# Kernel tuning notes

Hardware: AMD Instinct MI355X
Metric: run time of the kernel (lower is better)

Reference implementation:

```python
import jax, jax.numpy as jnp
import numpy as np

DIR_EDGES = [(0,1),(0,2),(0,3),(0,4),(0,13),(0,15),(3,5),(5,6),(4,7),(7,8),(1,9),(9,10),(2,11),(11,12),(13,14),(15,16)]
BP_EDGES = [(1,0),(1,2),(1,3),(1,4),(1,5)]
BODY_PARTS = [[13,14,15,16],[0,3,4],[1,9,10],[2,11,12],[5,6],[7,8]]
V1, V2 = 17, 6           # dir-vec graph nodes, body-part graph nodes
F1 = 16                  # st_gcn output channels
MAX_BP = 4               # max_body_part_edges
NOISE_DIM = 64
EPS = 1e-5


def build_A(num_node, edges, max_hop=2, center=0):
    """ST-GCN 'spatial' partition strategy -> (2*max_hop+1, V, V) float32."""
    adj = np.zeros((num_node, num_node))
    for i, j in edges:
        adj[i, j] = 1.0
        adj[j, i] = 1.0
    hop_dis = np.full((num_node, num_node), np.inf)
    powers = [np.linalg.matrix_power(adj + np.eye(num_node), d) for d in range(max_hop + 1)]
    arrive = np.stack(powers) > 0
    for d in range(max_hop, -1, -1):
        hop_dis[arrive[d]] = d
    adjacency = np.zeros((num_node, num_node))
    for hop in range(max_hop + 1):
        adjacency[hop_dis == hop] = 1.0
    Dl = adjacency.sum(0)
    Dn = np.zeros((num_node, num_node))
    for i in range(num_node):
        if Dl[i] > 0:
            Dn[i, i] = Dl[i] ** -1
    na = adjacency @ Dn
    parts = []
    for hop in range(max_hop + 1):
        a_root = np.zeros((num_node, num_node))
        a_close = np.zeros_like(a_root)
        a_far = np.zeros_like(a_root)
        for i in range(num_node):
            for j in range(num_node):
                if hop_dis[j, i] == hop:
                    if hop_dis[j, center] == hop_dis[i, center]:
                        a_root[j, i] = na[j, i]
                    elif hop_dis[j, center] > hop_dis[i, center]:
                        a_close[j, i] = na[j, i]
                    else:
                        a_far[j, i] = na[j, i]
        if hop == 0:
            parts.append(a_root)
        else:
            parts.append(a_root + a_close)
            parts.append(a_far)
    return np.stack(parts).astype(np.float32)


def _bn_params(k, c):
    k1, k2, k3, k4 = jax.random.split(k, 4)
    gamma = 1.0 + 0.1 * jax.random.normal(k1, (c,), dtype=jnp.float32)
    beta = 0.1 * jax.random.normal(k2, (c,), dtype=jnp.float32)
    mean = 0.1 * jax.random.normal(k3, (c,), dtype=jnp.float32)
    var = 1.0 + 0.1 * jax.random.uniform(k4, (c,), dtype=jnp.float32)
    return gamma, beta, mean, var


def setup_inputs() -> dict:
    key = jax.random.key(0)
    ks = jax.random.split(key, 12)
    n, t = 16, 2048
    poses = jax.random.normal(ks[0], (n, t, V1 * 3), dtype=jnp.float32)
    A1 = jnp.asarray(build_A(V1, DIR_EDGES, max_hop=2, center=0))  # (5,17,17)
    A2 = jnp.asarray(build_A(V2, BP_EDGES, max_hop=2, center=0))   # (5,6,6)
    K = 5
    w1 = 0.05 * jax.random.normal(ks[1], (F1 * K, 3, 9, 5), dtype=jnp.float32)
    b1 = 0.05 * jax.random.normal(ks[2], (F1 * K,), dtype=jnp.float32)
    w2 = 0.05 * jax.random.normal(ks[3], (F1 * K, MAX_BP * F1, 9, 3), dtype=jnp.float32)
    b2 = 0.05 * jax.random.normal(ks[4], (F1 * K,), dtype=jnp.float32)
    w3 = 0.05 * jax.random.normal(ks[5], (16, F1 * V2, 5), dtype=jnp.float32)
    b3 = 0.05 * jax.random.normal(ks[6], (16,), dtype=jnp.float32)
    w4 = 0.05 * jax.random.normal(ks[7], (NOISE_DIM, 16, 3), dtype=jnp.float32)
    b4 = 0.05 * jax.random.normal(ks[8], (NOISE_DIM,), dtype=jnp.float32)
    g1, be1, m1, v1 = _bn_params(ks[9], F1 * V1)
    g2, be2, m2, v2 = _bn_params(ks[10], F1 * V2)
    kk = jax.random.split(ks[11], 2)
    g3, be3, m3, v3 = _bn_params(kk[0], 16)
    g4, be4, m4, v4 = _bn_params(kk[1], NOISE_DIM)
    return dict(poses=poses, A1=A1, A2=A2, w1=w1, b1=b1, g1=g1, be1=be1, m1=m1, v1=v1,
                w2=w2, b2=b2, g2=g2, be2=be2, m2=m2, v2=v2,
                w3=w3, b3=b3, g3=g3, be3=be3, m3=m3, v3=v3,
                w4=w4, b4=b4, g4=g4, be4=be4, m4=m4, v4=v4)


def _bn(x, g, b, m, v):
    # x: (n, C, t), eval-mode BatchNorm1d
    s = (g * jax.lax.rsqrt(v + EPS))
    return (x - m[None, :, None]) * s[None, :, None] + b[None, :, None]


def _conv2d(x, w, b, pad):
    y = jax.lax.conv_general_dilated(x, w, (1, 1), [(pad[0], pad[0]), (pad[1], pad[1])],
                                     dimension_numbers=('NCHW', 'OIHW', 'NCHW'))
    return y + b[None, :, None, None]


def _conv1d(x, w, b, pad):
    y = jax.lax.conv_general_dilated(x, w, (1,), [(pad, pad)],
                                     dimension_numbers=('NCH', 'OIH', 'NCH'))
    return y + b[None, :, None]


def _leaky(x):
    return jax.nn.leaky_relu(x, 0.01)


def reference(poses, A1, A2, w1, b1, g1, be1, m1, v1, w2, b2, g2, be2, m2, v2,
              w3, b3, g3, be3, m3, v3, w4, b4, g4, be4, m4, v4):
    n, t, _ = poses.shape
    K = A1.shape[0]
    # (n, 3, t, V1)
    x = jnp.transpose(poses.reshape(n, t, V1, 3), (0, 3, 1, 2))
    # st_gcn1: 2D conv over (t, v) then graph-partition einsum
    y = _conv2d(x, w1, b1, (4, 2)).reshape(n, K, F1, t, V1)
    f1 = jnp.einsum('nkctv,kvw->nctw', y, A1)            # (n, F1, t, V1)
    # bn1 on flattened (F1*V1) channels
    z = jnp.transpose(f1, (0, 1, 3, 2)).reshape(n, F1 * V1, t)
    z = _bn(z, g1, be1, m1, v1)
    f1bn = jnp.transpose(z.reshape(n, F1, V1, t), (0, 1, 3, 2))  # (n, F1, t, V1)
    # body-part gather/pad assembly -> (n, t, MAX_BP*F1, V2)
    cols = []
    for idxs in BODY_PARTS:
        g = f1bn[:, :, :, jnp.asarray(idxs)]             # (n, F1, t, L)
        g = jnp.transpose(g, (0, 2, 1, 3)).reshape(n, t, -1)  # (n, t, F1*L)
        cols.append(jnp.pad(g, ((0, 0), (0, 0), (0, MAX_BP * F1 - g.shape[-1]))))
    f2_in = jnp.transpose(jnp.stack(cols, axis=-1), (0, 2, 1, 3))  # (n, 64, t, V2)
    # st_gcn2
    y2 = _conv2d(f2_in, w2, b2, (4, 1)).reshape(n, K, F1, t, V2)
    f2 = jnp.einsum('nkctv,kvw->nctw', y2, A2)           # (n, F1, t, V2)
    z2 = jnp.transpose(f2, (0, 1, 3, 2)).reshape(n, F1 * V2, t)
    z2 = _bn(z2, g2, be2, m2, v2)
    f2bn = jnp.transpose(z2.reshape(n, F1, V2, t), (0, 1, 3, 2))   # (n, F1, t, V2)
    # (n, F1*V2, t)
    f3_in = jnp.transpose(jnp.transpose(f2bn, (0, 2, 1, 3)).reshape(n, t, -1), (0, 2, 1))
    f3 = _leaky(_bn(_conv1d(f3_in, w3, b3, 2), g3, be3, m3, v3))
    f4 = _leaky(_bn(_conv1d(f3, w4, b4, 1), g4, be4, m4, v4))
    return jnp.transpose(f4, (0, 2, 1))                  # (n, t, noise_dim)
```

## Files before the change

kernel.cpp:

```cpp
#include <hip/hip_runtime.h>
#include <stdint.h>

typedef unsigned short u16;
typedef __attribute__((ext_vector_type(8))) __bf16 bf16x8;
typedef __attribute__((ext_vector_type(8))) u16 u16x8;
typedef __attribute__((ext_vector_type(4))) float f32x4;

#define T_LEN 2048
#define NB 16

__device__ __forceinline__ u16 f2bf(float f){
  uint32_t x = __builtin_bit_cast(uint32_t, f);
  x += 0x7FFFu + ((x >> 16) & 1u);
  return (u16)(x >> 16);
}

__constant__ int c_part[17] = {1,2,3,1,1,4,4,5,5,2,2,3,3,0,0,0,0};
__constant__ int c_pidx[17] = {0,0,0,1,2,0,1,0,1,1,2,1,2,0,1,2,3};
__constant__ int c_plen[17] = {3,3,3,3,3,2,2,2,2,3,3,3,3,4,4,4,4};

__global__ void conv_poses(const float* __restrict__ poses, u16* __restrict__ X0)
{
  int e = blockIdx.x * 256 + threadIdx.x;
  int row = e / 56, c = e - row * 56;
  u16 v = 0;
  if (c < 51) v = f2bf(poses[row * 51 + c]);
  X0[e] = v;
}

__global__ void prep_A(
  const float* __restrict__ w1, const float* __restrict__ A1, const float* __restrict__ g1, const float* __restrict__ v1,
  const float* __restrict__ w2, const float* __restrict__ A2, const float* __restrict__ g2, const float* __restrict__ v2,
  const float* __restrict__ w3, const float* __restrict__ g3, const float* __restrict__ v3,
  const float* __restrict__ w4, const float* __restrict__ g4, const float* __restrict__ v4,
  const float* b1, const float* be1, const float* m1,
  const float* b2, const float* be2, const float* m2,
  const float* b3, const float* be3, const float* m3,
  const float* b4, const float* be4, const float* m4,
  float* __restrict__ W1e, float* __restrict__ W1eT,
  float* __restrict__ W2e, float* __restrict__ W2eT,
  float* __restrict__ W3e, u16* __restrict__ W4f,
  float* bias1f, float* bias2f, float* bias3f, float* bias4f)
{
  const int bid = blockIdx.x;
  const int tid = threadIdx.x;
  if (bid < 488){
    int idx = bid * 256 + tid;
    if (idx < 124848){
      int p = idx / 459, rem = idx - p * 459;
      int d1 = rem / 51, u = rem - d1 * 51;
      int c = p / 17, w = p - c * 17;
      int uj = u / 3, ci = u - uj * 3;
      float val = 0.f;
      for (int kk = 0; kk < 5; ++kk)
        for (int dv = 0; dv < 5; ++dv){
          int v = uj - dv + 2;
          if (v >= 0 && v < 17)
            val += w1[(kk*16 + c)*135 + ci*45 + d1*5 + dv] * A1[kk*289 + v*17 + w];
        }
      val *= g1[p] * rsqrtf(v1[p] + 1e-5f);
      W1e[idx] = val;
      W1eT[(d1*51 + u)*272 + p] = val;
    }
  } else if (bid < 1406){
    int idx = (bid - 488) * 256 + tid;
    int o = idx / 2448, rem = idx - o * 2448;
    int d2 = rem / 272, pp = rem - d2 * 272;
    int c2 = o / 6, w2i = o - c2 * 6;
    int f = pp / 17, J = pp - f * 17;
    int pt = c_part[J];
    int ci = f * c_plen[J] + c_pidx[J];
    float val = 0.f;
    for (int kk = 0; kk < 5; ++kk)
      for (int dv = 0; dv < 3; ++dv){
        int v = pt - dv + 1;
        if (v >= 0 && v < 6)
          val += w2[(kk*16 + c2)*1728 + ci*27 + d2*3 + dv] * A2[kk*36 + v*6 + w2i];
      }
    val *= g2[o] * rsqrtf(v2[o] + 1e-5f);
    W2e[idx] = val;
    W2eT[(d2*272 + pp)*96 + o] = val;
  } else if (bid < 1436){
    int idx = (bid - 1406) * 256 + tid;
    int q = idx / 480, rem = idx - q * 480;
    int d3 = rem / 96, o = rem - d3 * 96;
    float s = g3[q] * rsqrtf(v3[q] + 1e-5f);
    W3e[idx] = s * w3[q*480 + o*5 + d3];
  } else if (bid < 1452){
    int i2 = (bid - 1436) * 256 + tid;
    int cw = i2 >> 6, kp = i2 & 63;
    int dt = kp >> 4, ch = kp & 15;
    float val = 0.f;
    if (dt < 3){
      float s = g4[cw] * rsqrtf(v4[cw] + 1e-5f);
      val = s * w4[cw*48 + ch*3 + dt];
    }
    int mt = cw >> 4, r = cw & 15, ks = kp >> 5, kq = kp & 31;
    W4f[(ks*4 + mt)*512 + ((kq>>3)*16 + r)*8 + (kq&7)] = f2bf(val);
  } else {
    int t2 = (bid - 1452) * 256 + tid;
    if (t2 < 272){
      int c = t2 / 17, w = t2 - c * 17;
      float beff = 0.f;
      for (int kk = 0; kk < 5; ++kk){
        float rs = 0.f;
        for (int v = 0; v < 17; ++v) rs += A1[kk*289 + v*17 + w];
        beff += b1[kk*16 + c] * rs;
      }
      float s = g1[t2] * rsqrtf(v1[t2] + 1e-5f);
      bias1f[t2] = s * (beff - m1[t2]) + be1[t2];
    } else if (t2 < 368){
      int cw = t2 - 272;
      int c = cw / 6, w = cw - c * 6;
      float beff = 0.f;
      for (int kk = 0; kk < 5; ++kk){
        float rs = 0.f;
        for (int v = 0; v < 6; ++v) rs += A2[kk*36 + v*6 + w];
        beff += b2[kk*16 + c] * rs;
      }
      float s = g2[cw] * rsqrtf(v2[cw] + 1e-5f);
      bias2f[cw] = s * (beff - m2[cw]) + be2[cw];
    } else if (t2 < 384){
      int o = t2 - 368;
      float s = g3[o] * rsqrtf(v3[o] + 1e-5f);
      bias3f[o] = s * (b3[o] - m3[o]) + be3[o];
    } else if (t2 < 448){
      int o = t2 - 384;
      float s = g4[o] * rsqrtf(v4[o] + 1e-5f);
      bias4f[o] = s * (b4[o] - m4[o]) + be4[o];
    }
  }
}

__global__ void prep_B(const float* __restrict__ W3e, const float* __restrict__ W2e,
                       const float* __restrict__ W2eT, const float* __restrict__ W1e,
                       const float* __restrict__ b2f, const float* __restrict__ b3f,
                       float* __restrict__ W32, float* __restrict__ W32ind,
                       u16* __restrict__ W1f, u16* __restrict__ W2f, u16* __restrict__ W3f)
{
  const int bid = blockIdx.x;
  const int tid = threadIdx.x;
  const int lane = tid & 63;
  const int h = tid >> 6;
  if (bid < 14144){
    int wid = bid * 4 + h;
    int b = wid / 272, p = wid - b * 272;
    int q = b / 13, d23 = b - q * 13;
    float accl = 0.f;
    for (int d3 = 0; d3 < 5; ++d3){
      int d2 = d23 - d3;
      if (d2 < 0 || d2 >= 9) continue;
      const float* w3r = W3e + q*480 + d3*96;
      const float* w2r = W2eT + (d2*272 + p)*96;
#pragma unroll
      for (int j = 0; j < 2; ++j){
        int o = lane + j*64;
        if (o < 96) accl += w3r[o] * w2r[o];
      }
    }
    for (int m = 32; m > 0; m >>= 1) accl += __shfl_xor(accl, m);
    if (lane == 0) W32[b*272 + p] = accl;
  } else if (bid < 14196){
    int wid = (bid - 14144) * 4 + h;
    int q = wid / 13, d23 = wid - q * 13;
    float accl = 0.f;
    int d3 = d23 - 4;
    if (d3 >= 0 && d3 < 5){
      const float* w3r = W3e + q*480 + d3*96;
#pragma unroll
      for (int j = 0; j < 2; ++j){
        int o = lane + j*64;
        if (o < 96) accl += w3r[o] * b2f[o];
      }
    }
    for (int m = 32; m > 0; m >>= 1) accl += __shfl_xor(accl, m);
    if (lane == 0){
      if (d23 == 6) accl += b3f[q];
      W32ind[wid] = accl;
    }
  } else if (bid < 14740){
    int idx = (bid - 14196) * 256 + tid;
    int cw = idx >> 9, kp = idx & 511;
    int dt = kp / 56, u = kp - dt * 56;
    float val = (dt < 9 && u < 51) ? W1e[(cw*9 + dt)*51 + u] : 0.f;
    int mt = cw >> 4, r = cw & 15, ks = kp >> 5, kq = kp & 31;
    W1f[(ks*17 + mt)*512 + ((kq>>3)*16 + r)*8 + (kq&7)] = f2bf(val);
  } else if (bid < 15676){
    int idx = (bid - 14740) * 256 + tid;
    int cw = idx / 2496, kp = idx - cw * 2496;
    int dt = kp / 272, pp = kp - dt * 272;
    float val = (dt < 9) ? W2e[(cw*9 + dt)*272 + pp] : 0.f;
    int mt = cw >> 4, r = cw & 15, ks = kp >> 5, kq = kp & 31;
    W2f[(ks*6 + mt)*512 + ((kq>>3)*16 + r)*8 + (kq&7)] = f2bf(val);
  } else {
    int idx = (bid - 15676) * 256 + tid;
    int cw = idx >> 9, kp = idx & 511;
    int dt = kp / 96, ch = kp - dt * 96;
    float val = (dt < 5) ? W3e[cw*480 + dt*96 + ch] : 0.f;
    int ks = kp >> 5, kq = kp & 31;
    W3f[ks*512 + ((kq>>3)*16 + cw)*8 + (kq&7)] = f2bf(val);
  }
}

__global__ void prep_C(const float* __restrict__ W32, const float* __restrict__ W32ind,
                       const float* __restrict__ W1eT, const float* __restrict__ b1f,
                       u16* __restrict__ WcfH, u16* __restrict__ WcfL,
                       float* __restrict__ biasC)
{
  const int tid = threadIdx.x;
  const int lane = tid & 63;
  const int h = tid >> 6;
  if (blockIdx.x == 4704){
    if (tid < 128){
      int kpi = 1176 + (tid >> 4), qq = tid & 15;
      int ks = kpi >> 5, kq = kpi & 31;
      int pos = ks*512 + ((kq>>3)*16 + qq)*8 + (kq&7);
      WcfH[pos] = 0; WcfL[pos] = 0;
    }
    for (int qi = 0; qi < 4; ++qi){
      int q = h*4 + qi;
      float accl = 0.f;
      for (int d23 = 0; d23 < 13; ++d23){
        const float* wrow = W32 + (q*13 + d23)*272;
#pragma unroll
        for (int j = 0; j < 5; ++j){
          int p = lane + j*64;
          if (p < 272) accl += wrow[p] * b1f[p];
        }
      }
      for (int m = 32; m > 0; m >>= 1) accl += __shfl_xor(accl, m);
      if (lane == 0){
        float ind = 0.f;
        for (int d23 = 0; d23 < 13; ++d23) ind += W32ind[q*13 + d23];
        biasC[q] = accl + ind;
      }
    }
    return;
  }
  int wid = blockIdx.x * 4 + h;
  int q = wid / 1176, rem = wid - q * 1176;
  int D = rem / 56, uu = rem - D * 56;
  float accl = 0.f;
  if (uu < 51){
    for (int d1 = 0; d1 < 9; ++d1){
      int d23 = D - d1;
      if (d23 < 0 || d23 >= 13) continue;
      const float* wrow = W32 + (q*13 + d23)*272;
      const float* w1r  = W1eT + (d1*51 + uu)*272;
#pragma unroll
      for (int j = 0; j < 5; ++j){
        int p = lane + j*64;
        if (p < 272) accl += wrow[p] * w1r[p];
      }
    }
  }
  for (int m = 32; m > 0; m >>= 1) accl += __shfl_xor(accl, m);
  if (lane == 0){
    int kp = D * 56 + uu;
    int ks = kp >> 5, kq = kp & 31;
    int pos = ks*512 + ((kq>>3)*16 + q)*8 + (kq&7);
    u16 hb = f2bf(accl);
    float hf = __builtin_bit_cast(float, (uint32_t)hb << 16);
    WcfH[pos] = hb;
    WcfL[pos] = f2bf(accl - hf);
  }
}

__launch_bounds__(256)
__global__ void fused_main(const u16* __restrict__ X0, const u16* __restrict__ WcfH,
                           const u16* __restrict__ WcfL, const float* __restrict__ biasC,
                           const u16* __restrict__ W4f, const float* __restrict__ bias4f,
                           const u16* __restrict__ W1f, const u16* __restrict__ W2f,
                           const u16* __restrict__ W3f,
                           const float* __restrict__ b1f, const float* __restrict__ b2f,
                           const float* __restrict__ b3f,
                           float* __restrict__ out)
{
  __shared__ __align__(16) u16 patch[69 * 56];
  __shared__ __align__(16) u16 X3L[48 * 16];
  __shared__ __align__(16) u16 xs [25 * 56];
  __shared__ __align__(16) u16 X1s[25 * 272];
  __shared__ __align__(16) u16 X2s[21 * 96];
  __shared__ __align__(16) u16 X3s[19 * 16];

  const int n  = blockIdx.y;
  const int tid = threadIdx.x;
  const int lane = tid & 63;
  const int h    = tid >> 6;
  const int q    = lane >> 4;
  const int l15  = lane & 15;

  if (blockIdx.x < 2){
    const int e = blockIdx.x;
    const int base1 = e ? (T_LEN - 14) : 0;
    const int off1 = e ? 0 : 4, off2 = e ? 0 : 2, off3 = e ? 0 : 1;

    for (int i = tid; i < 1140; i += 256){
      if (i < 850)        *reinterpret_cast<u16x8*>(&X1s[i*8]) = (u16x8)0;
      else if (i < 1102)  *reinterpret_cast<u16x8*>(&X2s[(i-850)*8]) = (u16x8)0;
      else                *reinterpret_cast<u16x8*>(&X3s[(i-1102)*8]) = (u16x8)0;
    }
    for (int idx = tid; idx < 25 * 7; idx += 256){
      int r = idx / 7, g = idx - r * 7;
      int t = base1 + r - 4;
      u16x8 v = (u16x8)0;
      if (t >= 0 && t < T_LEN)
        v = *reinterpret_cast<const u16x8*>(&X0[((size_t)n * T_LEN + t) * 56 + g * 8]);
      *reinterpret_cast<u16x8*>(&xs[r * 56 + g * 8]) = v;
    }
    __syncthreads();

    for (int mt = h; mt < 17; mt += 4){
      f32x4 acc = (f32x4){0.f,0.f,0.f,0.f};
      for (int ks = 0; ks < 16; ++ks){
        bf16x8 aF = *reinterpret_cast<const bf16x8*>(&W1f[(ks*17 + mt)*512 + lane*8]);
        int k0 = ks*32 + q*8;
        int dt = k0 / 56, rr = k0 - dt*56;
        bf16x8 bF = *reinterpret_cast<const bf16x8*>(&xs[(l15 + dt)*56 + rr]);
        acc = __builtin_amdgcn_mfma_f32_16x16x32_bf16(aF, bF, acc, 0, 0, 0);
      }
      if (l15 < 14){
        int chb = mt*16 + q*4;
        ushort4 o;
        o.x = f2bf(acc[0] + b1f[chb+0]); o.y = f2bf(acc[1] + b1f[chb+1]);
        o.z = f2bf(acc[2] + b1f[chb+2]); o.w = f2bf(acc[3] + b1f[chb+3]);
        *reinterpret_cast<ushort4*>(&X1s[(l15 + off1)*272 + chb]) = o;
      }
    }
    __syncthreads();

    for (int mt = h; mt < 6; mt += 4){
      f32x4 acc = (f32x4){0.f,0.f,0.f,0.f};
      for (int ks = 0; ks < 78; ++ks){
        bf16x8 aF = *reinterpret_cast<const bf16x8*>(&W2f[(ks*6 + mt)*512 + lane*8]);
        int k0 = ks*32 + q*8;
        int dt = k0 / 272, rr = k0 - dt*272;
        bf16x8 bF = *reinterpret_cast<const bf16x8*>(&X1s[(l15 + dt)*272 + rr]);
        acc = __builtin_amdgcn_mfma_f32_16x16x32_bf16(aF, bF, acc, 0, 0, 0);
      }
      if (l15 < 10){
        int chb = mt*16 + q*4;
        ushort4 o;
        o.x = f2bf(acc[0] + b2f[chb+0]); o.y = f2bf(acc[1] + b2f[chb+1]);
        o.z = f2bf(acc[2] + b2f[chb+2]); o.w = f2bf(acc[3] + b2f[chb+3]);
        *reinterpret_cast<ushort4*>(&X2s[(l15 + off2)*96 + chb]) = o;
      }
    }
    __syncthreads();

    if (h == 0){
      f32x4 acc = (f32x4){0.f,0.f,0.f,0.f};
      for (int ks = 0; ks < 16; ++ks){
        bf16x8 aF = *reinterpret_cast<const bf16x8*>(&W3f[ks*512 + lane*8]);
        int k0 = ks*32 + q*8;
        int dt = k0 / 96, rr = k0 - dt*96;
        bf16x8 bF = *reinterpret_cast<const bf16x8*>(&X2s[(l15 + dt)*96 + rr]);
        acc = __builtin_amdgcn_mfma_f32_16x16x32_bf16(aF, bF, acc, 0, 0, 0);
      }
      if (l15 < 8){
        float v0 = acc[0] + b3f[q*4+0], v1 = acc[1] + b3f[q*4+1];
        float v2 = acc[2] + b3f[q*4+2], v3 = acc[3] + b3f[q*4+3];
        v0 = v0 > 0.f ? v0 : 0.01f*v0; v1 = v1 > 0.f ? v1 : 0.01f*v1;
        v2 = v2 > 0.f ? v2 : 0.01f*v2; v3 = v3 > 0.f ? v3 : 0.01f*v3;
        ushort4 o; o.x = f2bf(v0); o.y = f2bf(v1); o.z = f2bf(v2); o.w = f2bf(v3);
        *reinterpret_cast<ushort4*>(&X3s[(l15 + off3)*16 + q*4]) = o;
      }
    }
    __syncthreads();

    {
      f32x4 acc = (f32x4){0.f,0.f,0.f,0.f};
      for (int ks = 0; ks < 2; ++ks){
        bf16x8 aF = *reinterpret_cast<const bf16x8*>(&W4f[(ks*4 + h)*512 + lane*8]);
        int k0 = ks*32 + q*8;
        int dt2 = k0 >> 4, ch0 = k0 & 15;
        bf16x8 bF = *reinterpret_cast<const bf16x8*>(&X3s[(l15 + dt2)*16 + ch0]);
        acc = __builtin_amdgcn_mfma_f32_16x16x32_bf16(aF, bF, acc, 0, 0, 0);
      }
      if (l15 < 7){
        int chb = h*16 + q*4;
        int t = (e ? (T_LEN - 7) : 0) + l15;
        float v0 = acc[0] + bias4f[chb+0], v1 = acc[1] + bias4f[chb+1];
        float v2 = acc[2] + bias4f[chb+2], v3 = acc[3] + bias4f[chb+3];
        v0 = v0 > 0.f ? v0 : 0.01f*v0; v1 = v1 > 0.f ? v1 : 0.01f*v1;
        v2 = v2 > 0.f ? v2 : 0.01f*v2; v3 = v3 > 0.f ? v3 : 0.01f*v3;
        float4 o; o.x = v0; o.y = v1; o.z = v2; o.w = v3;
        *reinterpret_cast<float4*>(&out[((size_t)n * T_LEN + t) * 64 + chb]) = o;
      }
    }
    return;
  }

  const int t0 = (blockIdx.x - 2) * 32;

  for (int idx = tid; idx < 69 * 7; idx += 256){
    int row = idx / 7, g = idx - row * 7;
    int ts = t0 + row - 18;
    u16x8 v = (u16x8)0;
    if (ts >= 0 && ts < T_LEN)
      v = *reinterpret_cast<const u16x8*>(&X0[((size_t)n * T_LEN + ts) * 56 + g * 8]);
    *reinterpret_cast<u16x8*>(&patch[row * 56 + g * 8]) = v;
  }
  __syncthreads();

  if (h < 3){
    f32x4 a0 = (f32x4){0.f, 0.f, 0.f, 0.f};
    bf16x8 aH[2], aL[2], bF[2];
    const u16* bp0 = patch + (16 * h + l15) * 56;
    auto load3 = [&](int buf, int ks){
      const int k0 = ks * 32 + q * 8;
      const int D = k0 / 56, rr = k0 - D * 56;
      aH[buf] = *reinterpret_cast<const bf16x8*>(WcfH + ks * 512 + lane * 8);
      aL[buf] = *reinterpret_cast<const bf16x8*>(WcfL + ks * 512 + lane * 8);
      bF[buf] = *reinterpret_cast<const bf16x8*>(bp0 + D * 56 + rr);
    };
    load3(0, 0);
    for (int ks = 0; ks < 37; ++ks){
      const int cur = ks & 1;
      if (ks + 1 < 37) load3(cur ^ 1, ks + 1);
      a0 = __builtin_amdgcn_mfma_f32_16x16x32_bf16(aH[cur], bF[cur], a0, 0, 0, 0);
      a0 = __builtin_amdgcn_mfma_f32_16x16x32_bf16(aL[cur], bF[cur], a0, 0, 0, 0);
    }
    const float bc0 = biasC[q*4+0], bc1 = biasC[q*4+1], bc2 = biasC[q*4+2], bc3 = biasC[q*4+3];
    int trow = 16 * h + l15;
    int t = t0 - 8 + trow;
    float v0 = a0[0]+bc0, v1 = a0[1]+bc1, v2 = a0[2]+bc2, v3 = a0[3]+bc3;
    v0 = v0 > 0.f ? v0 : 0.01f*v0; v1 = v1 > 0.f ? v1 : 0.01f*v1;
    v2 = v2 > 0.f ? v2 : 0.01f*v2; v3 = v3 > 0.f ? v3 : 0.01f*v3;
    if (t < 0 || t >= T_LEN){ v0 = v1 = v2 = v3 = 0.f; }
    ushort4 o; o.x = f2bf(v0); o.y = f2bf(v1); o.z = f2bf(v2); o.w = f2bf(v3);
    *reinterpret_cast<ushort4*>(&X3L[trow * 16 + q * 4]) = o;
  }
  __syncthreads();

  {
    f32x4 acc[2];
#pragma unroll
    for (int j = 0; j < 2; ++j) acc[j] = (f32x4){0.f, 0.f, 0.f, 0.f};
    bf16x8 aF[2], bF[2][2];
    auto load4 = [&](int buf, int ks){
      const int k0 = ks * 32 + q * 8;
      const int dt2 = k0 >> 4, ch0 = k0 & 15;
      aF[buf] = *reinterpret_cast<const bf16x8*>(W4f + (ks * 4 + h) * 512 + lane * 8);
#pragma unroll
      for (int j = 0; j < 2; ++j)
        bF[buf][j] = *reinterpret_cast<const bf16x8*>(&X3L[(j * 16 + l15 + dt2 + 7) * 16 + ch0]);
    };
    load4(0, 0); load4(1, 1);
#pragma unroll
    for (int j = 0; j < 2; ++j)
      acc[j] = __builtin_amdgcn_mfma_f32_16x16x32_bf16(aF[0], bF[0][j], acc[j], 0, 0, 0);
#pragma unroll
    for (int j = 0; j < 2; ++j)
      acc[j] = __builtin_amdgcn_mfma_f32_16x16x32_bf16(aF[1], bF[1][j], acc[j], 0, 0, 0);

    const int chb = h * 16 + q * 4;
    const float c0 = bias4f[chb+0], c1 = bias4f[chb+1], c2 = bias4f[chb+2], c3 = bias4f[chb+3];
#pragma unroll
    for (int j = 0; j < 2; ++j){
      const int t = t0 + j * 16 + l15;
      float v0 = acc[j][0]+c0, v1 = acc[j][1]+c1, v2 = acc[j][2]+c2, v3 = acc[j][3]+c3;
      v0 = v0 > 0.f ? v0 : 0.01f*v0; v1 = v1 > 0.f ? v1 : 0.01f*v1;
      v2 = v2 > 0.f ? v2 : 0.01f*v2; v3 = v3 > 0.f ? v3 : 0.01f*v3;
      if (t >= 7 && t < T_LEN - 7){
        float4 o; o.x = v0; o.y = v1; o.z = v2; o.w = v3;
        *reinterpret_cast<float4*>(&out[((size_t)n * T_LEN + t) * 64 + chb]) = o;
      }
    }
  }
}

extern "C" void kernel_launch(void* const* d_in, const int* in_sizes, int n_in,
                              void* d_out, int out_size, void* d_ws, size_t ws_size,
                              hipStream_t stream)
{
  const float* poses = (const float*)d_in[0];
  const float* A1  = (const float*)d_in[1];
  const float* A2  = (const float*)d_in[2];
  const float* w1  = (const float*)d_in[3];
  const float* b1  = (const float*)d_in[4];
  const float* g1  = (const float*)d_in[5];
  const float* be1 = (const float*)d_in[6];
  const float* m1  = (const float*)d_in[7];
  const float* v1  = (const float*)d_in[8];
  const float* w2  = (const float*)d_in[9];
  const float* b2  = (const float*)d_in[10];
  const float* g2  = (const float*)d_in[11];
  const float* be2 = (const float*)d_in[12];
  const float* m2  = (const float*)d_in[13];
  const float* v2  = (const float*)d_in[14];
  const float* w3  = (const float*)d_in[15];
  const float* b3  = (const float*)d_in[16];
  const float* g3  = (const float*)d_in[17];
  const float* be3 = (const float*)d_in[18];
  const float* m3  = (const float*)d_in[19];
  const float* v3  = (const float*)d_in[20];
  const float* w4  = (const float*)d_in[21];
  const float* b4  = (const float*)d_in[22];
  const float* g4  = (const float*)d_in[23];
  const float* be4 = (const float*)d_in[24];
  const float* m4  = (const float*)d_in[25];
  const float* v4  = (const float*)d_in[26];

  uint8_t* ws = (uint8_t*)d_ws;
  size_t off = 0;
  auto alloc = [&](size_t bytes) -> void* {
    void* p = ws + off;
    off += (bytes + 255) & ~(size_t)255;
    return p;
  };
  u16*   X0    = (u16*)  alloc((size_t)NB * T_LEN * 56 * 2);
  float* W1e   = (float*)alloc(124848 * 4);
  float* W1eT  = (float*)alloc(124848 * 4);
  float* W2e   = (float*)alloc(235008 * 4);
  float* W2eT  = (float*)alloc(235008 * 4);
  float* W3e   = (float*)alloc(7680 * 4);
  u16*   W4f   = (u16*)  alloc(4096 * 2);
  float* b1f   = (float*)alloc(272 * 4);
  float* b2f   = (float*)alloc(96 * 4);
  float* b3f   = (float*)alloc(16 * 4);
  float* b4f   = (float*)alloc(64 * 4);
  float* W32   = (float*)alloc(208 * 272 * 4);
  float* W32i  = (float*)alloc(208 * 4);
  u16*   WcfH  = (u16*)  alloc(37 * 512 * 2);
  u16*   WcfL  = (u16*)  alloc(37 * 512 * 2);
  float* biasC = (float*)alloc(16 * 4);
  u16*   W1f   = (u16*)  alloc(139264 * 2);
  u16*   W2f   = (u16*)  alloc(239616 * 2);
  u16*   W3f   = (u16*)  alloc(8192 * 2);

  hipLaunchKernelGGL(conv_poses, dim3(7168), dim3(256), 0, stream, poses, X0);
  hipLaunchKernelGGL(prep_A, dim3(1454), dim3(256), 0, stream,
                     w1, A1, g1, v1, w2, A2, g2, v2, w3, g3, v3, w4, g4, v4,
                     b1, be1, m1, b2, be2, m2, b3, be3, m3, b4, be4, m4,
                     W1e, W1eT, W2e, W2eT, W3e, W4f,
                     b1f, b2f, b3f, b4f);
  hipLaunchKernelGGL(prep_B, dim3(15708), dim3(256), 0, stream,
                     W3e, W2e, W2eT, W1e, b2f, b3f, W32, W32i, W1f, W2f, W3f);
  hipLaunchKernelGGL(prep_C, dim3(4705), dim3(256), 0, stream,
                     W32, W32i, W1eT, b1f, WcfH, WcfL, biasC);
  hipLaunchKernelGGL(fused_main, dim3(66, 16), dim3(256), 0, stream,
                     X0, WcfH, WcfL, biasC, W4f, b4f, W1f, W2f, W3f,
                     b1f, b2f, b3f, (float*)d_out);
}
```

Before: 189.4 us.

## Merge weight-prep kernels into one launch and restructure W32/Wc composition

Folds the pose conversion, the effective-weight construction and the W32 composition into a single prep kernel, so the swizzled bf16 fragments are written directly and the W1e/W2e/W2eT/W3e intermediates disappear. W32 is now computed per column in shared memory, recomputing W2 and W3 slices locally. prep_Wc has each wave produce four output columns, reusing each W32 row load across them. This cuts launches and global round-trips, at the cost of redundant per-block recomputation and more shared memory in the merged kernel.

After: 222.8 us. 1.18x slower.

```diff
diff --git a/kernel.cpp b/kernel.cpp
--- a/kernel.cpp
+++ b/kernel.cpp
@@ -19,33 +19,41 @@
 __constant__ int c_pidx[17] = {0,0,0,1,2,0,1,0,1,1,2,1,2,0,1,2,3};
 __constant__ int c_plen[17] = {3,3,3,3,3,2,2,2,2,3,3,3,3,4,4,4,4};
 
-__global__ void conv_poses(const float* __restrict__ poses, u16* __restrict__ X0)
+__launch_bounds__(256)
+__global__ void prep_all(
+  const float* __restrict__ poses, const float* __restrict__ A1, const float* __restrict__ A2,
+  const float* __restrict__ w1, const float* __restrict__ b1, const float* __restrict__ g1,
+  const float* __restrict__ be1, const float* __restrict__ m1, const float* __restrict__ v1,
+  const float* __restrict__ w2, const float* __restrict__ b2, const float* __restrict__ g2,
+  const float* __restrict__ be2, const float* __restrict__ m2, const float* __restrict__ v2,
+  const float* __restrict__ w3, const float* __restrict__ b3, const float* __restrict__ g3,
+  const float* __restrict__ be3, const float* __restrict__ m3, const float* __restrict__ v3,
+  const float* __restrict__ w4, const float* __restrict__ b4, const float* __restrict__ g4,
+  const float* __restrict__ be4, const float* __restrict__ m4, const float* __restrict__ v4,
+  u16* __restrict__ X0, float* __restrict__ W1eT,
+  u16* __restrict__ W1f, u16* __restrict__ W2f, u16* __restrict__ W3f, u16* __restrict__ W4f,
+  float* __restrict__ b1f, float* __restrict__ b2f, float* __restrict__ b3f, float* __restrict__ b4f,
+  float* __restrict__ W32, float* __restrict__ W32i)
 {
-  int e = blockIdx.x * 256 + threadIdx.x;
-  int row = e / 56, c = e - row * 56;
-  u16 v = 0;
-  if (c < 51) v = f2bf(poses[row * 51 + c]);
-  X0[e] = v;
-}
-
-__global__ void prep_A(
-  const float* __restrict__ w1, const float* __restrict__ A1, const float* __restrict__ g1, const float* __restrict__ v1,
-  const float* __restrict__ w2, const float* __restrict__ A2, const float* __restrict__ g2, const float* __restrict__ v2,
-  const float* __restrict__ w3, const float* __restrict__ g3, const float* __restrict__ v3,
-  const float* __restrict__ w4, const float* __restrict__ g4, const float* __restrict__ v4,
-  const float* b1, const float* be1, const float* m1,
-  const float* b2, const float* be2, const float* m2,
-  const float* b3, const float* be3, const float* m3,
-  const float* b4, const float* be4, const float* m4,
-  float* __restrict__ W1e, float* __restrict__ W1eT,
-  float* __restrict__ W2e, float* __restrict__ W2eT,
-  float* __restrict__ W3e, u16* __restrict__ W4f,
-  float* bias1f, float* bias2f, float* bias3f, float* bias4f)
-{
-  const int bid = blockIdx.x;
+  __shared__ float W2L[864];
+  __shared__ float W3L[7680];
+  __shared__ float b2L[96];
+  __shared__ float b3L[16];
+  __shared__ float s3L[16];
+
+  const int vb  = blockIdx.x;
   const int tid = threadIdx.x;
-  if (bid < 488){
-    int idx = bid * 256 + tid;
+  const int lane = tid & 63;
+  const int h    = tid >> 6;
+
+  if (vb < 7168){
+    int e = vb * 256 + tid;
+    int row = e / 56, c = e - row * 56;
+    u16 v = 0;
+    if (c < 51) v = f2bf(poses[row * 51 + c]);
+    X0[e] = v;
+  } else if (vb < 7656){
+    int idx = (vb - 7168) * 256 + tid;
     if (idx < 124848){
       int p = idx / 459, rem = idx - p * 459;
       int d1 = rem / 51, u = rem - d1 * 51;
@@ -59,11 +67,13 @@
             val += w1[(kk*16 + c)*135 + ci*45 + d1*5 + dv] * A1[kk*289 + v*17 + w];
         }
       val *= g1[p] * rsqrtf(v1[p] + 1e-5f);
-      W1e[idx] = val;
       W1eT[(d1*51 + u)*272 + p] = val;
-    }
-  } else if (bid < 1406){
-    int idx = (bid - 488) * 256 + tid;
+      int kp = d1*56 + u;
+      int mt = p >> 4, r = p & 15, ks = kp >> 5, kq = kp & 31;
+      W1f[(ks*17 + mt)*512 + ((kq>>3)*16 + r)*8 + (kq&7)] = f2bf(val);
+    }
+  } else if (vb < 8574){
+    int idx = (vb - 7656) * 256 + tid;
     int o = idx / 2448, rem = idx - o * 2448;
     int d2 = rem / 272, pp = rem - d2 * 272;
     int c2 = o / 6, w2i = o - c2 * 6;
@@ -78,16 +88,22 @@
           val += w2[(kk*16 + c2)*1728 + ci*27 + d2*3 + dv] * A2[kk*36 + v*6 + w2i];
       }
     val *= g2[o] * rsqrtf(v2[o] + 1e-5f);
-    W2e[idx] = val;
-    W2eT[(d2*272 + pp)*96 + o] = val;
-  } else if (bid < 1436){
-    int idx = (bid - 1406) * 256 + tid;
-    int q = idx / 480, rem = idx - q * 480;
-    int d3 = rem / 96, o = rem - d3 * 96;
-    float s = g3[q] * rsqrtf(v3[q] + 1e-5f);
-    W3e[idx] = s * w3[q*480 + o*5 + d3];
-  } else if (bid < 1452){
-    int i2 = (bid - 1436) * 256 + tid;
+    int kp = d2*272 + pp;
+    int mt = o >> 4, r = o & 15, ks = kp >> 5, kq = kp & 31;
+    W2f[(ks*6 + mt)*512 + ((kq>>3)*16 + r)*8 + (kq&7)] = f2bf(val);
+  } else if (vb < 8606){
+    int idx = (vb - 8574) * 256 + tid;
+    int cw = idx >> 9, kp = idx & 511;
+    int dt = kp / 96, ch = kp - dt * 96;
+    float val = 0.f;
+    if (dt < 5){
+      float s = g3[cw] * rsqrtf(v3[cw] + 1e-5f);
+      val = s * w3[cw*480 + ch*5 + dt];
+    }
+    int ks = kp >> 5, kq = kp & 31;
+    W3f[ks*512 + ((kq>>3)*16 + cw)*8 + (kq&7)] = f2bf(val);
+  } else if (vb < 8622){
+    int i2 = (vb - 8606) * 256 + tid;
     int cw = i2 >> 6, kp = i2 & 63;
     int dt = kp >> 4, ch = kp & 15;
     float val = 0.f;
@@ -97,8 +113,8 @@
     }
     int mt = cw >> 4, r = cw & 15, ks = kp >> 5, kq = kp & 31;
     W4f[(ks*4 + mt)*512 + ((kq>>3)*16 + r)*8 + (kq&7)] = f2bf(val);
-  } else {
-    int t2 = (bid - 1452) * 256 + tid;
+  } else if (vb < 8624){
+    int t2 = (vb - 8622) * 256 + tid;
     if (t2 < 272){
       int c = t2 / 17, w = t2 - c * 17;
       float beff = 0.f;
@@ -108,7 +124,7 @@
         beff += b1[kk*16 + c] * rs;
       }
       float s = g1[t2] * rsqrtf(v1[t2] + 1e-5f);
-      bias1f[t2] = s * (beff - m1[t2]) + be1[t2];
+      b1f[t2] = s * (beff - m1[t2]) + be1[t2];
     } else if (t2 < 368){
       int cw = t2 - 272;
       int c = cw / 6, w = cw - c * 6;
@@ -119,98 +135,116 @@
         beff += b2[kk*16 + c] * rs;
       }
       float s = g2[cw] * rsqrtf(v2[cw] + 1e-5f);
-      bias2f[cw] = s * (beff - m2[cw]) + be2[cw];
+      b2f[cw] = s * (beff - m2[cw]) + be2[cw];
     } else if (t2 < 384){
       int o = t2 - 368;
       float s = g3[o] * rsqrtf(v3[o] + 1e-5f);
-      bias3f[o] = s * (b3[o] - m3[o]) + be3[o];
+      b3f[o] = s * (b3[o] - m3[o]) + be3[o];
     } else if (t2 < 448){
       int o = t2 - 384;
       float s = g4[o] * rsqrtf(v4[o] + 1e-5f);
-      bias4f[o] = s * (b4[o] - m4[o]) + be4[o];
+      b4f[o] = s * (b4[o] - m4[o]) + be4[o];
+    }
+  } else if (vb < 8681){
+    int i = (vb - 8624) * 256 + tid;
+    if (i < 14416){
+      int cw = i / 53, j = i - cw * 53;
+      int kp = (j < 45) ? ((j/5)*56 + 51 + (j - (j/5)*5)) : (504 + (j - 45));
+      int mt = cw >> 4, r = cw & 15, ks = kp >> 5, kq = kp & 31;
+      W1f[(ks*17 + mt)*512 + ((kq>>3)*16 + r)*8 + (kq&7)] = 0;
+    }
+  } else if (vb < 8699){
+    int i = (vb - 8681) * 256 + tid;
+    int cw = i / 48, kp = 2448 + (i - cw * 48);
+    int mt = cw >> 4, r = cw & 15, ks = kp >> 5, kq = kp & 31;
+    W2f[(ks*6 + mt)*512 + ((kq>>3)*16 + r)*8 + (kq&7)] = 0;
+  } else if (vb < 8971){
+    const int p = vb - 8699;
+    const int f = p / 17, J = p - f * 17;
+    const int pt = c_part[J];
+    const int ci = f * c_plen[J] + c_pidx[J];
+    for (int t = tid; t < 864; t += 256){
+      int o = t / 9, d2 = t - o * 9;
+      int c2 = o / 6, w2i = o - c2 * 6;
+      float val = 0.f;
+      for (int kk = 0; kk < 5; ++kk)
+        for (int dv = 0; dv < 3; ++dv){
+          int v = pt - dv + 1;
+          if (v >= 0 && v < 6)
+            val += w2[(kk*16 + c2)*1728 + ci*27 + d2*3 + dv] * A2[kk*36 + v*6 + w2i];
+        }
+      val *= g2[o] * rsqrtf(v2[o] + 1e-5f);
+      W2L[o*9 + d2] = val;
+    }
+    for (int t = tid; t < 7680; t += 256){
+      int qq = t / 480, r = t - qq * 480;
+      int d3 = r / 96, o = r - d3 * 96;
+      W3L[t] = g3[qq] * rsqrtf(v3[qq] + 1e-5f) * w3[qq*480 + o*5 + d3];
+    }
+    __syncthreads();
+    for (int ob = h; ob < 208; ob += 4){
+      int qq = ob / 13, d23 = ob - qq * 13;
+      float accl = 0.f;
+      for (int d3 = 0; d3 < 5; ++d3){
+        int d2 = d23 - d3;
+        if (d2 < 0 || d2 >= 9) continue;
+#pragma unroll
+        for (int j = 0; j < 2; ++j){
+          int o = lane + j*64;
+          if (o < 96) accl += W3L[qq*480 + d3*96 + o] * W2L[o*9 + d2];
+        }
+      }
+      for (int m = 32; m > 0; m >>= 1) accl += __shfl_xor(accl, m);
+      if (lane == 0) W32[ob*272 + p] = accl;
+    }
+  } else {
+    if (tid < 96){
+      int o = tid, c2 = o / 6, w2i = o - c2 * 6;
+      float beff = 0.f;
+      for (int kk = 0; kk < 5; ++kk){
+        float rs = 0.f;
+        for (int v = 0; v < 6; ++v) rs += A2[kk*36 + v*6 + w2i];
+        beff += b2[kk*16 + c2] * rs;
+      }
+      float s = g2[o] * rsqrtf(v2[o] + 1e-5f);
+      b2L[o] = s * (beff - m2[o]) + be2[o];
+    } else if (tid < 112){
+      int qq = tid - 96;
+      float s = g3[qq] * rsqrtf(v3[qq] + 1e-5f);
+      s3L[qq] = s;
+      b3L[qq] = s * (b3[qq] - m3[qq]) + be3[qq];
+    }
+    __syncthreads();
+    for (int ob = h; ob < 208; ob += 4){
+      int qq = ob / 13, d23 = ob - qq * 13;
+      float accl = 0.f;
+      int d3 = d23 - 4;
+      if (d3 >= 0 && d3 < 5){
+#pragma unroll
+        for (int j = 0; j < 2; ++j){
+          int o = lane + j*64;
+          if (o < 96) accl += s3L[qq] * w3[qq*480 + o*5 + d3] * b2L[o];
+        }
+      }
+      for (int m = 32; m > 0; m >>= 1) accl += __shfl_xor(accl, m);
+      if (lane == 0){
+        if (d23 == 6) accl += b3L[qq];
+        W32i[ob] = accl;
+      }
     }
   }
 }
 
-__global__ void prep_B(const float* __restrict__ W3e, const float* __restrict__ W2e,
-                       const float* __restrict__ W2eT, const float* __restrict__ W1e,
-                       const float* __restrict__ b2f, const float* __restrict__ b3f,
-                       float* __restrict__ W32, float* __restrict__ W32ind,
-                       u16* __restrict__ W1f, u16* __restrict__ W2f, u16* __restrict__ W3f)
-{
-  const int bid = blockIdx.x;
-  const int tid = threadIdx.x;
-  const int lane = tid & 63;
-  const int h = tid >> 6;
-  if (bid < 14144){
-    int wid = bid * 4 + h;
-    int b = wid / 272, p = wid - b * 272;
-    int q = b / 13, d23 = b - q * 13;
-    float accl = 0.f;
-    for (int d3 = 0; d3 < 5; ++d3){
-      int d2 = d23 - d3;
-      if (d2 < 0 || d2 >= 9) continue;
-      const float* w3r = W3e + q*480 + d3*96;
-      const float* w2r = W2eT + (d2*272 + p)*96;
-#pragma unroll
-      for (int j = 0; j < 2; ++j){
-        int o = lane + j*64;
-        if (o < 96) accl += w3r[o] * w2r[o];
-      }
-    }
-    for (int m = 32; m > 0; m >>= 1) accl += __shfl_xor(accl, m);
-    if (lane == 0) W32[b*272 + p] = accl;
-  } else if (bid < 14196){
-    int wid = (bid - 14144) * 4 + h;
-    int q = wid / 13, d23 = wid - q * 13;
-    float accl = 0.f;
-    int d3 = d23 - 4;
-    if (d3 >= 0 && d3 < 5){
-      const float* w3r = W3e + q*480 + d3*96;
-#pragma unroll
-      for (int j = 0; j < 2; ++j){
-        int o = lane + j*64;
-        if (o < 96) accl += w3r[o] * b2f[o];
-      }
-    }
-    for (int m = 32; m > 0; m >>= 1) accl += __shfl_xor(accl, m);
-    if (lane == 0){
-      if (d23 == 6) accl += b3f[q];
-      W32ind[wid] = accl;
-    }
-  } else if (bid < 14740){
-    int idx = (bid - 14196) * 256 + tid;
-    int cw = idx >> 9, kp = idx & 511;
-    int dt = kp / 56, u = kp - dt * 56;
-    float val = (dt < 9 && u < 51) ? W1e[(cw*9 + dt)*51 + u] : 0.f;
-    int mt = cw >> 4, r = cw & 15, ks = kp >> 5, kq = kp & 31;
-    W1f[(ks*17 + mt)*512 + ((kq>>3)*16 + r)*8 + (kq&7)] = f2bf(val);
-  } else if (bid < 15676){
-    int idx = (bid - 14740) * 256 + tid;
-    int cw = idx / 2496, kp = idx - cw * 2496;
-    int dt = kp / 272, pp = kp - dt * 272;
-    float val = (dt < 9) ? W2e[(cw*9 + dt)*272 + pp] : 0.f;
-    int mt = cw >> 4, r = cw & 15, ks = kp >> 5, kq = kp & 31;
-    W2f[(ks*6 + mt)*512 + ((kq>>3)*16 + r)*8 + (kq&7)] = f2bf(val);
-  } else {
-    int idx = (bid - 15676) * 256 + tid;
-    int cw = idx >> 9, kp = idx & 511;
-    int dt = kp / 96, ch = kp - dt * 96;
-    float val = (dt < 5) ? W3e[cw*480 + dt*96 + ch] : 0.f;
-    int ks = kp >> 5, kq = kp & 31;
-    W3f[ks*512 + ((kq>>3)*16 + cw)*8 + (kq&7)] = f2bf(val);
-  }
-}
-
-__global__ void prep_C(const float* __restrict__ W32, const float* __restrict__ W32ind,
-                       const float* __restrict__ W1eT, const float* __restrict__ b1f,
-                       u16* __restrict__ WcfH, u16* __restrict__ WcfL,
-                       float* __restrict__ biasC)
+__launch_bounds__(256)
+__global__ void prep_Wc(const float* __restrict__ W32, const float* __restrict__ W32i,
+                        const float* __restrict__ W1eT, const float* __restrict__ b1f,
+                        u16* __restrict__ WcfH, u16* __restrict__ WcfL,
+                        float* __restrict__ biasC)
 {
   const int tid = threadIdx.x;
   const int lane = tid & 63;
   const int h = tid >> 6;
-  if (blockIdx.x == 4704){
+  if (blockIdx.x == 1176){
     if (tid < 128){
       int kpi = 1176 + (tid >> 4), qq = tid & 15;
       int ks = kpi >> 5, kq = kpi & 31;
@@ -218,10 +252,10 @@
       WcfH[pos] = 0; WcfL[pos] = 0;
     }
     for (int qi = 0; qi < 4; ++qi){
-      int q = h*4 + qi;
+      int qq = h*4 + qi;
       float accl = 0.f;
       for (int d23 = 0; d23 < 13; ++d23){
-        const float* wrow = W32 + (q*13 + d23)*272;
+        const float* wrow = W32 + (qq*13 + d23)*272;
 #pragma unroll
         for (int j = 0; j < 5; ++j){
           int p = lane + j*64;
@@ -231,38 +265,51 @@
       for (int m = 32; m > 0; m >>= 1) accl += __shfl_xor(accl, m);
       if (lane == 0){
         float ind = 0.f;
-        for (int d23 = 0; d23 < 13; ++d23) ind += W32ind[q*13 + d23];
-        biasC[q] = accl + ind;
+        for (int d23 = 0; d23 < 13; ++d23) ind += W32i[qq*13 + d23];
+        biasC[qq] = accl + ind;
       }
     }
     return;
   }
-  int wid = blockIdx.x * 4 + h;
-  int q = wid / 1176, rem = wid - q * 1176;
-  int D = rem / 56, uu = rem - D * 56;
-  float accl = 0.f;
-  if (uu < 51){
-    for (int d1 = 0; d1 < 9; ++d1){
-      int d23 = D - d1;
-      if (d23 < 0 || d23 >= 13) continue;
-      const float* wrow = W32 + (q*13 + d23)*272;
-      const float* w1r  = W1eT + (d1*51 + uu)*272;
-#pragma unroll
-      for (int j = 0; j < 5; ++j){
-        int p = lane + j*64;
-        if (p < 272) accl += wrow[p] * w1r[p];
-      }
-    }
-  }
-  for (int m = 32; m > 0; m >>= 1) accl += __shfl_xor(accl, m);
+  int g = blockIdx.x * 4 + h;
+  int q = g / 294, rem = g - q * 294;
+  int D = rem / 14, u4 = (rem - D * 14) * 4;
+  float a0=0.f, a1=0.f, a2=0.f, a3=0.f;
+  for (int d1 = 0; d1 < 9; ++d1){
+    int d23 = D - d1;
+    if (d23 < 0 || d23 >= 13) continue;
+    const float* wrow = W32 + (q*13 + d23)*272;
+    const float* w1b  = W1eT + (d1*51)*272;
+#pragma unroll
+    for (int j = 0; j < 5; ++j){
+      int p = lane + j*64;
+      if (p < 272){
+        float wr = wrow[p];
+        if (u4+0 < 51) a0 += wr * w1b[(u4+0)*272 + p];
+        if (u4+1 < 51) a1 += wr * w1b[(u4+1)*272 + p];
+        if (u4+2 < 51) a2 += wr * w1b[(u4+2)*272 + p];
+        if (u4+3 < 51) a3 += wr * w1b[(u4+3)*272 + p];
+      }
+    }
+  }
+  for (int m = 32; m > 0; m >>= 1){
+    a0 += __shfl_xor(a0, m); a1 += __shfl_xor(a1, m);
+    a2 += __shfl_xor(a2, m); a3 += __shfl_xor(a3, m);
+  }
   if (lane == 0){
-    int kp = D * 56 + uu;
-    int ks = kp >> 5, kq = kp & 31;
-    int pos = ks*512 + ((kq>>3)*16 + q)*8 + (kq&7);
-    u16 hb = f2bf(accl);
-    float hf = __builtin_bit_cast(float, (uint32_t)hb << 16);
-    WcfH[pos] = hb;
-    WcfL[pos] = f2bf(accl - hf);
+    float accs[4] = {a0, a1, a2, a3};
+#pragma unroll
+    for (int mI = 0; mI < 4; ++mI){
+      int uu = u4 + mI;
+      float a = (uu < 51) ? accs[mI] : 0.f;
+      int kp = D*56 + uu;
+      int ks = kp >> 5, kq = kp & 31;
+      int pos = ks*512 + ((kq>>3)*16 + q)*8 + (kq&7);
+      u16 hb = f2bf(a);
+      float hf = __builtin_bit_cast(float, (uint32_t)hb << 16);
+      WcfH[pos] = hb;
+      WcfL[pos] = f2bf(a - hf);
+    }
   }
 }
 
@@ -510,11 +557,10 @@
     return p;
   };
   u16*   X0    = (u16*)  alloc((size_t)NB * T_LEN * 56 * 2);
-  float* W1e   = (float*)alloc(124848 * 4);
   float* W1eT  = (float*)alloc(124848 * 4);
-  float* W2e   = (float*)alloc(235008 * 4);
-  float* W2eT  = (float*)alloc(235008 * 4);
-  float* W3e   = (float*)alloc(7680 * 4);
+  u16*   W1f   = (u16*)  alloc(139264 * 2);
+  u16*   W2f   = (u16*)  alloc(239616 * 2);
+  u16*   W3f   = (u16*)  alloc(8192 * 2);
   u16*   W4f   = (u16*)  alloc(4096 * 2);
   float* b1f   = (float*)alloc(272 * 4);
   float* b2f   = (float*)alloc(96 * 4);
@@ -525,19 +571,16 @@
   u16*   WcfH  = (u16*)  alloc(37 * 512 * 2);
   u16*   WcfL  = (u16*)  alloc(37 * 512 * 2);
   float* biasC = (float*)alloc(16 * 4);
-  u16*   W1f   = (u16*)  alloc(139264 * 2);
-  u16*   W2f   = (u16*)  alloc(239616 * 2);
-  u16*   W3f   = (u16*)  alloc(8192 * 2);
-
-  hipLaunchKernelGGL(conv_poses, dim3(7168), dim3(256), 0, stream, poses, X0);
-  hipLaunchKernelGGL(prep_A, dim3(1454), dim3(256), 0, stream,
-                     w1, A1, g1, v1, w2, A2, g2, v2, w3, g3, v3, w4, g4, v4,
-                     b1, be1, m1, b2, be2, m2, b3, be3, m3, b4, be4, m4,
-                     W1e, W1eT, W2e, W2eT, W3e, W4f,
-                     b1f, b2f, b3f, b4f);
-  hipLaunchKernelGGL(prep_B, dim3(15708), dim3(256), 0, stream,
-                     W3e, W2e, W2eT, W1e, b2f, b3f, W32, W32i, W1f, W2f, W3f);
-  hipLaunchKernelGGL(prep_C, dim3(4705), dim3(256), 0, stream,
+
+  hipLaunchKernelGGL(prep_all, dim3(8972), dim3(256), 0, stream,
+                     poses, A1, A2,
+                     w1, b1, g1, be1, m1, v1,
+                     w2, b2, g2, be2, m2, v2,
+                     w3, b3, g3, be3, m3, v3,
+                     w4, b4, g4, be4, m4, v4,
+                     X0, W1eT, W1f, W2f, W3f, W4f,
+                     b1f, b2f, b3f, b4f, W32, W32i);
+  hipLaunchKernelGGL(prep_Wc, dim3(1177), dim3(256), 0, stream,
                      W32, W32i, W1eT, b1f, WcfH, WcfL, biasC);
   hipLaunchKernelGGL(fused_main, dim3(66, 16), dim3(256), 0, stream,
                      X0, WcfH, WcfL, biasC, W4f, b4f, W1f, W2f, W3f,
```
